# Performance work log

Measured on AMD Instinct MI355X. Metric: run time of the kernel, lower is better.

Reference implementation:

```python
import jax, jax.numpy as jnp
import numpy as np

B, M, IN, HID, A = 4096, 64, 3, 128, 64
D = 50.0                       # waveguide_bound
H_CONST = 5.0
PMAX = 10.0 ** (30 / 10 - 3)   # = 1.0 (30 dBm in Watts)
C_LIGHT = 3.0e8
FC = 6.0e9
DELTA_MIN = (C_LIGHT / FC) / 2.0  # 0.025
ALPHA = 0.2                    # LeakyReLU slope


def setup_inputs() -> dict:
    key = jax.random.key(0)
    ks = jax.random.split(key, 9)
    s = lambda k, sh: (jax.random.normal(k, sh, jnp.float32) * 0.1)
    return {
        "users": jax.random.normal(ks[0], (B, M, IN), jnp.float32),
        "W1": s(ks[1], (IN, HID)),    # GAT layer 1 projection (applied as h @ W)
        "a1": s(ks[2], (2 * HID,)),   # GAT layer 1 attention vector
        "W2": s(ks[3], (HID, HID)),   # GAT layer 2 projection
        "a2": s(ks[4], (2 * HID,)),
        "mw1": s(ks[5], (HID, 32)),   # MLP Linear(hidden, 32)
        "mb1": jnp.zeros((32,), jnp.float32),
        "mw2": s(ks[6], (32, 2 * A)), # MLP Linear(32, 2*num_antennas)
        "mb2": jnp.zeros((2 * A,), jnp.float32),
    }


def gat_layer(h, W, a):
    # Wh: [B, M, d]
    Wh = h @ W
    d = W.shape[1]
    # e[b,i,j] = leakyrelu( cat(Wh_i, Wh_j) . a ) = leakyrelu( Wh_i.a[:d] + Wh_j.a[d:] )
    si = Wh @ a[:d]          # [B, M]
    sj = Wh @ a[d:]          # [B, M]
    e = jax.nn.leaky_relu(si[:, :, None] + sj[:, None, :], ALPHA)  # [B, M, M]
    attn = jax.nn.softmax(e, axis=-1)  # softmax over neighbors j (dropout p=0 -> identity)
    h_prime = jnp.einsum('bij,bjd->bid', attn, Wh)
    return jax.nn.elu(h_prime)


def reference(users, W1, a1, W2, a2, mw1, mb1, mw2, mb2):
    h = gat_layer(users, W1, a1)
    h = gat_layer(h, W2, a2)
    pooled = jnp.max(h, axis=1)                      # [B, hidden]
    readout = jax.nn.relu(pooled @ mw1 + mb1) @ mw2 + mb2  # [B, 2A]
    raw_delta, raw_power = readout[:, :A], readout[:, A:]
    eps = 1e-6
    raw_delta = jax.nn.relu(raw_delta) + eps
    raw_power = jax.nn.relu(raw_power) + eps
    Bmax = 2.0 * D - (A - 1) * DELTA_MIN
    delta = Bmax * raw_delta / (jnp.sum(raw_delta, axis=1, keepdims=True) + eps)
    power = PMAX * raw_power / (jnp.sum(raw_power, axis=1, keepdims=True) + eps)
    return power, delta
```

## Files before the change

### kernel.cpp

```cpp
#include <hip/hip_runtime.h>

#define NBATCH 4096
#define OUT2 (NBATCH * 64)

typedef _Float16 f16;
typedef __attribute__((ext_vector_type(8))) _Float16 f16x8;
typedef __attribute__((ext_vector_type(4))) _Float16 f16x4;
typedef __attribute__((ext_vector_type(4))) float f32x4;

__device__ __forceinline__ float lrelu(float x) { return fmaxf(x, 0.2f * x); }
__device__ __forceinline__ float elu1(float x)  { return x > 0.0f ? x : __expf(x) - 1.0f; }
__device__ __forceinline__ void lds_fence() {
    asm volatile("s_waitcnt lgkmcnt(0)" ::: "memory");
}

__global__ void prep(const float* __restrict__ W2, const float* __restrict__ W1,
                     const float* __restrict__ a1, const float* __restrict__ a2,
                     f16* __restrict__ w2b, float* __restrict__ w1a, f16* __restrict__ w2ab) {
    const int flat = blockIdx.x * 256 + threadIdx.x;
    const int slot = flat >> 3, j = flat & 7;
    const int F2T = slot >> 8, kf = (slot >> 6) & 3, ln = slot & 63;
    const int lq = ln >> 4, lr = ln & 15;
    w2b[flat] = (f16)W2[(kf * 32 + lq * 8 + j) * 128 + F2T * 16 + lr];
    if (flat < 2048) {
        const int ks = flat >> 9, ln2 = (flat >> 3) & 63, jj = flat & 7;
        const int k = ks * 32 + ((ln2 >> 4) & 3) * 8 + jj;
        const int n = ln2 & 15;
        float v = 0.f;
        if (n < 2) {
            const float* av = a2 + n * 128;
            for (int f2 = 0; f2 < 128; ++f2) v = fmaf(W2[k * 128 + f2], av[f2], v);
        }
        w2ab[flat] = (f16)v;
    }
    if (flat >= 16381) {
        const int c = flat - 16381;
        float si = 0.f, sj = 0.f;
        for (int f = 0; f < 128; ++f) {
            const float w = W1[c * 128 + f];
            si = fmaf(w, a1[f], si);
            sj = fmaf(w, a1[128 + f], sj);
        }
        w1a[c] = si; w1a[3 + c] = sj;
    }
}

__global__ __launch_bounds__(256, 2)
void gat_kernel(const float* __restrict__ users,
                const float* __restrict__ W1,
                const f16* __restrict__ w2b,
                const float* __restrict__ w1a,
                const f16* __restrict__ w2ab,
                const float* __restrict__ mw1,
                const float* __restrict__ mb1,
                const float* __restrict__ mw2,
                const float* __restrict__ mb2,
                float* __restrict__ out)
{
    const int wid  = threadIdx.x >> 6;
    const int b    = blockIdx.x * 4 + wid;
    const int lane = threadIdx.x & 63;
    const int lr   = lane & 15;
    const int lq   = lane >> 4;

    __shared__ __align__(16) char smem[4 * 9344];
    char*  sw    = smem + wid * 9344;
    f16*   sMain = (f16*)sw;
    float* sSi   = (float*)(sw + 8192);
    float* sSj   = (float*)(sw + 8448);
    float* sPool = (float*)(sw + 8704);
    float* sHid  = (float*)(sw + 9216);

    const float* u = users + b * 192;

    {
        const float x = u[lane * 3], y = u[lane * 3 + 1], z = u[lane * 3 + 2];
        sSi[lane] = fmaf(x, w1a[0], fmaf(y, w1a[1], z * w1a[2]));
        sSj[lane] = fmaf(x, w1a[3], fmaf(y, w1a[4], z * w1a[5]));
    }
    lds_fence();

    f16x8 bfr[4];
    {
        float sjv[16];
        *(float4*)&sjv[0]  = *(const float4*)&sSj[lq * 8];
        *(float4*)&sjv[4]  = *(const float4*)&sSj[lq * 8 + 4];
        *(float4*)&sjv[8]  = *(const float4*)&sSj[32 + lq * 8];
        *(float4*)&sjv[12] = *(const float4*)&sSj[32 + lq * 8 + 4];
        f16x8 ap[4][2];
        #pragma unroll
        for (int mt = 0; mt < 4; ++mt) {
            const float si = sSi[mt * 16 + lr];
            float pv[16];
            float lsum = 0.f;
            #pragma unroll
            for (int jj = 0; jj < 8; ++jj) {
                const float t0 = si + sjv[jj];
                const float t1 = si + sjv[8 + jj];
                const float p0 = __expf(lrelu(t0));
                const float p1 = __expf(lrelu(t1));
                pv[jj] = p0; pv[8 + jj] = p1;
                lsum += p0 + p1;
            }
            lsum += __shfl_xor(lsum, 16, 64);
            lsum += __shfl_xor(lsum, 32, 64);
            const float inv = 1.0f / lsum;
            #pragma unroll
            for (int jj = 0; jj < 8; ++jj) {
                ap[mt][0][jj] = (f16)(pv[jj] * inv);
                ap[mt][1][jj] = (f16)(pv[8 + jj] * inv);
            }
        }
        f16x8 af2[2];
        #pragma unroll
        for (int ks = 0; ks < 2; ++ks) {
            #pragma unroll
            for (int jj = 0; jj < 8; ++jj) {
                const int node = ks * 32 + lq * 8 + jj;
                af2[ks][jj] = (lr < 3) ? (f16)u[node * 3 + lr] : (f16)0.f;
            }
        }
        #pragma unroll
        for (int nt = 0; nt < 4; ++nt) {
            f32x4 d1 = (f32x4){0.f, 0.f, 0.f, 0.f};
            d1 = __builtin_amdgcn_mfma_f32_16x16x32_f16(af2[0], ap[nt][0], d1, 0, 0, 0);
            d1 = __builtin_amdgcn_mfma_f32_16x16x32_f16(af2[1], ap[nt][1], d1, 0, 0, 0);
            const float c0 = __shfl(d1[0], lr, 64);
            const float c1 = __shfl(d1[1], lr, 64);
            const float c2 = __shfl(d1[2], lr, 64);
            #pragma unroll
            for (int jj = 0; jj < 8; ++jj) bfr[nt][jj] = (f16)0.f;
            if (lq == 0) {
                bfr[nt][0] = (f16)c0; bfr[nt][1] = (f16)c1; bfr[nt][2] = (f16)c2;
            }
        }
    }

    f16x8 hf[4][4];
    #pragma unroll
    for (int h = 0; h < 2; ++h) {
        #pragma unroll
        for (int ftl = 0; ftl < 4; ++ftl) {
            f16x8 af3;
            #pragma unroll
            for (int jj = 0; jj < 8; ++jj) af3[jj] = (f16)0.f;
            if (lq == 0) {
                #pragma unroll
                for (int jj = 0; jj < 3; ++jj)
                    af3[jj] = (f16)W1[jj * 128 + (h * 4 + ftl) * 16 + lr];
            }
            #pragma unroll
            for (int nt = 0; nt < 4; ++nt) {
                f32x4 acc = (f32x4){0.f, 0.f, 0.f, 0.f};
                acc = __builtin_amdgcn_mfma_f32_16x16x32_f16(af3, bfr[nt], acc, 0, 0, 0);
                f16x4 hv;
                #pragma unroll
                for (int r = 0; r < 4; ++r) hv[r] = (f16)elu1(acc[r]);
                const int n = nt * 16 + lr;
                const int gg = 2 * ftl + (lq >> 1);
                *(f16x4*)&sMain[n * 64 + ((gg ^ (n & 7)) << 3) + ((lq & 1) * 4)] = hv;
            }
        }
        lds_fence();
        #pragma unroll
        for (int nt = 0; nt < 4; ++nt) {
            const int n = nt * 16 + lr;
            #pragma unroll
            for (int ksl = 0; ksl < 2; ++ksl)
                hf[nt][h * 2 + ksl] =
                    *(const f16x8*)&sMain[n * 64 + (((ksl * 4 + lq) ^ (n & 7)) << 3)];
        }
        lds_fence();
    }

    {
        f32x4 sacc[4];
        #pragma unroll
        for (int mt = 0; mt < 4; ++mt) sacc[mt] = (f32x4){0.f, 0.f, 0.f, 0.f};
        #pragma unroll
        for (int ks = 0; ks < 4; ++ks) {
            f16x8 bsw = *(const f16x8*)(w2ab + (ks * 64 + lane) * 8);
            #pragma unroll
            for (int mt = 0; mt < 4; ++mt)
                sacc[mt] = __builtin_amdgcn_mfma_f32_16x16x32_f16(hf[mt][ks], bsw, sacc[mt], 0, 0, 0);
        }
        if (lr < 2) {
            float* dst = (lr == 0) ? sSi : sSj;
            #pragma unroll
            for (int mt = 0; mt < 4; ++mt)
                #pragma unroll
                for (int r = 0; r < 4; ++r)
                    dst[mt * 16 + lq * 4 + r] = sacc[mt][r];
        }
    }
    lds_fence();

    f16x8 bp[4][2];
    {
        float sjv[16];
        *(float4*)&sjv[0]  = *(const float4*)&sSj[lq * 8];
        *(float4*)&sjv[4]  = *(const float4*)&sSj[lq * 8 + 4];
        *(float4*)&sjv[8]  = *(const float4*)&sSj[32 + lq * 8];
        *(float4*)&sjv[12] = *(const float4*)&sSj[32 + lq * 8 + 4];
        #pragma unroll
        for (int mt = 0; mt < 4; ++mt) {
            const float si = sSi[mt * 16 + lr];
            float pv[16];
            float lsum = 0.f;
            #pragma unroll
            for (int jj = 0; jj < 8; ++jj) {
                const float t0 = si + sjv[jj];
                const float t1 = si + sjv[8 + jj];
                const float p0 = __expf(lrelu(t0));
                const float p1 = __expf(lrelu(t1));
                pv[jj] = p0; pv[8 + jj] = p1;
                lsum += p0 + p1;
            }
            lsum += __shfl_xor(lsum, 16, 64);
            lsum += __shfl_xor(lsum, 32, 64);
            const float inv = 1.0f / lsum;
            #pragma unroll
            for (int jj = 0; jj < 8; ++jj) {
                bp[mt][0][jj] = (f16)(pv[jj] * inv);
                bp[mt][1][jj] = (f16)(pv[8 + jj] * inv);
            }
        }
    }

    int fst[4];
    #pragma unroll
    for (int nt = 0; nt < 4; ++nt) {
        const int gg = nt * 2 + (lq >> 1);
        fst[nt] = lr * 64 + ((gg ^ (lr & 7)) << 3) + ((lq & 1) * 4);
    }
    const int er0 = lr * 64 + ((lq ^ (lr & 7)) << 3);
    const int er1 = lr * 64 + (((4 + lq) ^ (lr & 7)) << 3);

    {
        f16x8 bw2[4];
        #pragma unroll
        for (int kf = 0; kf < 4; ++kf)
            bw2[kf] = *(const f16x8*)(w2b + ((0 * 4 + kf) * 64 + lane) * 8);
        #pragma unroll
        for (int nt = 0; nt < 4; ++nt) {
            f32x4 acc = (f32x4){0.f, 0.f, 0.f, 0.f};
            #pragma unroll
            for (int kf = 0; kf < 4; ++kf)
                acc = __builtin_amdgcn_mfma_f32_16x16x32_f16(hf[nt][kf], bw2[kf], acc, 0, 0, 0);
            f16x4 hv;
            #pragma unroll
            for (int r = 0; r < 4; ++r) hv[r] = (f16)acc[r];
            *(f16x4*)&sMain[fst[nt]] = hv;
        }
    }
    lds_fence();

    #pragma unroll 1
    for (int ft = 0; ft < 8; ++ft) {
        f16* rb = sMain + ((ft & 1) << 10);
        if (ft < 7) {
            f16* wb = sMain + (((ft + 1) & 1) << 10);
            f16x8 bw2[4];
            #pragma unroll
            for (int kf = 0; kf < 4; ++kf)
                bw2[kf] = *(const f16x8*)(w2b + (((ft + 1) * 4 + kf) * 64 + lane) * 8);
            #pragma unroll
            for (int nt = 0; nt < 4; ++nt) {
                f32x4 acc = (f32x4){0.f, 0.f, 0.f, 0.f};
                #pragma unroll
                for (int kf = 0; kf < 4; ++kf)
                    acc = __builtin_amdgcn_mfma_f32_16x16x32_f16(hf[nt][kf], bw2[kf], acc, 0, 0, 0);
                f16x4 hv;
                #pragma unroll
                for (int r = 0; r < 4; ++r) hv[r] = (f16)acc[r];
                *(f16x4*)&wb[fst[nt]] = hv;
            }
        }

        f16x8 bh0 = *(const f16x8*)&rb[er0];
        f16x8 bh1 = *(const f16x8*)&rb[er1];
        float mx = -1e30f;
        #pragma unroll
        for (int mt = 0; mt < 4; ++mt) {
            f32x4 acc = (f32x4){0.f, 0.f, 0.f, 0.f};
            acc = __builtin_amdgcn_mfma_f32_16x16x32_f16(bp[mt][0], bh0, acc, 0, 0, 0);
            acc = __builtin_amdgcn_mfma_f32_16x16x32_f16(bp[mt][1], bh1, acc, 0, 0, 0);
            mx = fmaxf(mx, fmaxf(fmaxf(acc[0], acc[1]), fmaxf(acc[2], acc[3])));
        }
        mx = fmaxf(mx, __shfl_xor(mx, 16, 64));
        mx = fmaxf(mx, __shfl_xor(mx, 32, 64));
        if (lane < 16) sPool[ft * 16 + lane] = elu1(mx);
        lds_fence();
    }

    {
        const int o = lane & 31, hh = lane >> 5;
        float s0 = 0.f;
        #pragma unroll 8
        for (int kk = 0; kk < 64; ++kk) {
            const int c = hh * 64 + kk;
            s0 = fmaf(sPool[c], mw1[c * 32 + o], s0);
        }
        s0 += __shfl_xor(s0, 32, 64);
        if (lane < 32) sHid[lane] = fmaxf(s0 + mb1[o], 0.0f);
    }
    lds_fence();
    {
        float sA = mb2[lane], sB = mb2[64 + lane];
        #pragma unroll 8
        for (int q = 0; q < 32; ++q) {
            const float wA = mw2[q * 128 + lane];
            const float wB = mw2[q * 128 + 64 + lane];
            const float h0 = sHid[q];
            sA = fmaf(h0, wA, sA);  sB = fmaf(h0, wB, sB);
        }
        float rA = fmaxf(sA, 0.0f) + 1e-6f, rB = fmaxf(sB, 0.0f) + 1e-6f;
        float uA = rA, uB = rB;
        #pragma unroll
        for (int m = 1; m < 64; m <<= 1) {
            uA += __shfl_xor(uA, m, 64);  uB += __shfl_xor(uB, m, 64);
        }
        out[b * 64 + lane]        = rB / (uB + 1e-6f);
        out[OUT2 + b * 64 + lane] = 98.425f * rA / (uA + 1e-6f);
    }
}

extern "C" void kernel_launch(void* const* d_in, const int* in_sizes, int n_in,
                              void* d_out, int out_size, void* d_ws, size_t ws_size,
                              hipStream_t stream) {
    const float* users = (const float*)d_in[0];
    const float* W1    = (const float*)d_in[1];
    const float* a1    = (const float*)d_in[2];
    const float* W2    = (const float*)d_in[3];
    const float* a2    = (const float*)d_in[4];
    const float* mw1   = (const float*)d_in[5];
    const float* mb1   = (const float*)d_in[6];
    const float* mw2   = (const float*)d_in[7];
    const float* mb2   = (const float*)d_in[8];
    float* out = (float*)d_out;

    f16*   w2b  = (f16*)d_ws;
    float* w1a  = (float*)((char*)d_ws + 32768);
    f16*   w2ab = (f16*)((char*)d_ws + 32800);

    prep<<<64, 256, 0, stream>>>(W2, W1, a1, a2, w2b, w1a, w2ab);
    gat_kernel<<<NBATCH / 4, 256, 0, stream>>>(users, W1, w2b, w1a, w2ab,
                                               mw1, mb1, mw2, mb2, out);
}
```

Before: 114.7 us.

## Replace LDS transpose staging with register shuffles between MFMA stages

```diff
diff --git a/kernel.cpp b/kernel.cpp
--- a/kernel.cpp
+++ b/kernel.cpp
@@ -5,13 +5,35 @@
 
 typedef _Float16 f16;
 typedef __attribute__((ext_vector_type(8))) _Float16 f16x8;
-typedef __attribute__((ext_vector_type(4))) _Float16 f16x4;
 typedef __attribute__((ext_vector_type(4))) float f32x4;
 
 __device__ __forceinline__ float lrelu(float x) { return fmaxf(x, 0.2f * x); }
 __device__ __forceinline__ float elu1(float x)  { return x > 0.0f ? x : __expf(x) - 1.0f; }
 __device__ __forceinline__ void lds_fence() {
     asm volatile("s_waitcnt lgkmcnt(0)" ::: "memory");
+}
+__device__ __forceinline__ unsigned pk2(float a, float b) {
+    union { f16 h[2]; unsigned u; } t;
+    t.h[0] = (f16)a; t.h[1] = (f16)b;
+    return t.u;
+}
+__device__ __forceinline__ f16x8 xpose(unsigned p0l, unsigned p0h,
+                                       unsigned p1l, unsigned p1h,
+                                       int s0, int s1, bool hiSel) {
+    const unsigned a0l = (unsigned)__shfl((int)p0l, s0, 64);
+    const unsigned a0h = (unsigned)__shfl((int)p0h, s0, 64);
+    const unsigned b0l = (unsigned)__shfl((int)p0l, s1, 64);
+    const unsigned b0h = (unsigned)__shfl((int)p0h, s1, 64);
+    const unsigned a1l = (unsigned)__shfl((int)p1l, s0, 64);
+    const unsigned a1h = (unsigned)__shfl((int)p1h, s0, 64);
+    const unsigned b1l = (unsigned)__shfl((int)p1l, s1, 64);
+    const unsigned b1h = (unsigned)__shfl((int)p1h, s1, 64);
+    union { unsigned u[4]; f16x8 v; } o;
+    o.u[0] = hiSel ? a1l : a0l;
+    o.u[1] = hiSel ? a1h : a0h;
+    o.u[2] = hiSel ? b1l : b0l;
+    o.u[3] = hiSel ? b1h : b0h;
+    return o.v;
 }
 
 __global__ void prep(const float* __restrict__ W2, const float* __restrict__ W1,
@@ -62,14 +84,16 @@
     const int lane = threadIdx.x & 63;
     const int lr   = lane & 15;
     const int lq   = lane >> 4;
-
-    __shared__ __align__(16) char smem[4 * 9344];
-    char*  sw    = smem + wid * 9344;
-    f16*   sMain = (f16*)sw;
-    float* sSi   = (float*)(sw + 8192);
-    float* sSj   = (float*)(sw + 8448);
-    float* sPool = (float*)(sw + 8704);
-    float* sHid  = (float*)(sw + 9216);
+    const int s0   = (lane & 15) | ((lane & 16) << 1);
+    const int s1   = s0 + 16;
+    const bool hiSel = (lane & 32) != 0;
+
+    __shared__ __align__(16) char smem[4 * 1280];
+    char*  sw    = smem + wid * 1280;
+    float* sSi   = (float*)(sw);
+    float* sSj   = (float*)(sw + 256);
+    float* sPool = (float*)(sw + 512);
+    float* sHid  = (float*)(sw + 1024);
 
     const float* u = users + b * 192;
 
@@ -95,10 +119,8 @@
             float lsum = 0.f;
             #pragma unroll
             for (int jj = 0; jj < 8; ++jj) {
-                const float t0 = si + sjv[jj];
-                const float t1 = si + sjv[8 + jj];
-                const float p0 = __expf(lrelu(t0));
-                const float p1 = __expf(lrelu(t1));
+                const float p0 = __expf(lrelu(si + sjv[jj]));
+                const float p1 = __expf(lrelu(si + sjv[8 + jj]));
                 pv[jj] = p0; pv[8 + jj] = p1;
                 lsum += p0 + p1;
             }
@@ -140,37 +162,34 @@
     #pragma unroll
     for (int h = 0; h < 2; ++h) {
         #pragma unroll
-        for (int ftl = 0; ftl < 4; ++ftl) {
-            f16x8 af3;
-            #pragma unroll
-            for (int jj = 0; jj < 8; ++jj) af3[jj] = (f16)0.f;
-            if (lq == 0) {
+        for (int ksl = 0; ksl < 2; ++ksl) {
+            f32x4 acc[4][2];
+            #pragma unroll
+            for (int tp = 0; tp < 2; ++tp) {
+                const int ftl = 2 * ksl + tp;
+                f16x8 af3;
                 #pragma unroll
-                for (int jj = 0; jj < 3; ++jj)
-                    af3[jj] = (f16)W1[jj * 128 + (h * 4 + ftl) * 16 + lr];
+                for (int jj = 0; jj < 8; ++jj) af3[jj] = (f16)0.f;
+                if (lq == 0) {
+                    #pragma unroll
+                    for (int jj = 0; jj < 3; ++jj)
+                        af3[jj] = (f16)W1[jj * 128 + (h * 4 + ftl) * 16 + lr];
+                }
+                #pragma unroll
+                for (int nt = 0; nt < 4; ++nt) {
+                    acc[nt][tp] = (f32x4){0.f, 0.f, 0.f, 0.f};
+                    acc[nt][tp] = __builtin_amdgcn_mfma_f32_16x16x32_f16(af3, bfr[nt], acc[nt][tp], 0, 0, 0);
+                }
             }
             #pragma unroll
             for (int nt = 0; nt < 4; ++nt) {
-                f32x4 acc = (f32x4){0.f, 0.f, 0.f, 0.f};
-                acc = __builtin_amdgcn_mfma_f32_16x16x32_f16(af3, bfr[nt], acc, 0, 0, 0);
-                f16x4 hv;
-                #pragma unroll
-                for (int r = 0; r < 4; ++r) hv[r] = (f16)elu1(acc[r]);
-                const int n = nt * 16 + lr;
-                const int gg = 2 * ftl + (lq >> 1);
-                *(f16x4*)&sMain[n * 64 + ((gg ^ (n & 7)) << 3) + ((lq & 1) * 4)] = hv;
-            }
-        }
-        lds_fence();
-        #pragma unroll
-        for (int nt = 0; nt < 4; ++nt) {
-            const int n = nt * 16 + lr;
-            #pragma unroll
-            for (int ksl = 0; ksl < 2; ++ksl)
-                hf[nt][h * 2 + ksl] =
-                    *(const f16x8*)&sMain[n * 64 + (((ksl * 4 + lq) ^ (n & 7)) << 3)];
-        }
-        lds_fence();
+                const unsigned p0l = pk2(elu1(acc[nt][0][0]), elu1(acc[nt][0][1]));
+                const unsigned p0h = pk2(elu1(acc[nt][0][2]), elu1(acc[nt][0][3]));
+                const unsigned p1l = pk2(elu1(acc[nt][1][0]), elu1(acc[nt][1][1]));
+                const unsigned p1h = pk2(elu1(acc[nt][1][2]), elu1(acc[nt][1][3]));
+                hf[nt][h * 2 + ksl] = xpose(p0l, p0h, p1l, p1h, s0, s1, hiSel);
+            }
+        }
     }
 
     {
@@ -184,6 +203,7 @@
             for (int mt = 0; mt < 4; ++mt)
                 sacc[mt] = __builtin_amdgcn_mfma_f32_16x16x32_f16(hf[mt][ks], bsw, sacc[mt], 0, 0, 0);
         }
+        lds_fence();
         if (lr < 2) {
             float* dst = (lr == 0) ? sSi : sSj;
             #pragma unroll
@@ -209,10 +229,8 @@
             float lsum = 0.f;
             #pragma unroll
             for (int jj = 0; jj < 8; ++jj) {
-                const float t0 = si + sjv[jj];
-                const float t1 = si + sjv[8 + jj];
-                const float p0 = __expf(lrelu(t0));
-                const float p1 = __expf(lrelu(t1));
+                const float p0 = __expf(lrelu(si + sjv[jj]));
+                const float p1 = __expf(lrelu(si + sjv[8 + jj]));
                 pv[jj] = p0; pv[8 + jj] = p1;
                 lsum += p0 + p1;
             }
@@ -227,58 +245,25 @@
         }
     }
 
-    int fst[4];
-    #pragma unroll
-    for (int nt = 0; nt < 4; ++nt) {
-        const int gg = nt * 2 + (lq >> 1);
-        fst[nt] = lr * 64 + ((gg ^ (lr & 7)) << 3) + ((lq & 1) * 4);
-    }
-    const int er0 = lr * 64 + ((lq ^ (lr & 7)) << 3);
-    const int er1 = lr * 64 + (((4 + lq) ^ (lr & 7)) << 3);
-
-    {
+    #pragma unroll 1
+    for (int ft = 0; ft < 8; ++ft) {
         f16x8 bw2[4];
         #pragma unroll
         for (int kf = 0; kf < 4; ++kf)
-            bw2[kf] = *(const f16x8*)(w2b + ((0 * 4 + kf) * 64 + lane) * 8);
+            bw2[kf] = *(const f16x8*)(w2b + ((ft * 4 + kf) * 64 + lane) * 8);
+        unsigned pkq[4][2];
         #pragma unroll
         for (int nt = 0; nt < 4; ++nt) {
             f32x4 acc = (f32x4){0.f, 0.f, 0.f, 0.f};
             #pragma unroll
             for (int kf = 0; kf < 4; ++kf)
                 acc = __builtin_amdgcn_mfma_f32_16x16x32_f16(hf[nt][kf], bw2[kf], acc, 0, 0, 0);
-            f16x4 hv;
-            #pragma unroll
-            for (int r = 0; r < 4; ++r) hv[r] = (f16)acc[r];
-            *(f16x4*)&sMain[fst[nt]] = hv;
-        }
-    }
-    lds_fence();
-
-    #pragma unroll 1
-    for (int ft = 0; ft < 8; ++ft) {
-        f16* rb = sMain + ((ft & 1) << 10);
-        if (ft < 7) {
-            f16* wb = sMain + (((ft + 1) & 1) << 10);
-            f16x8 bw2[4];
-            #pragma unroll
-            for (int kf = 0; kf < 4; ++kf)
-                bw2[kf] = *(const f16x8*)(w2b + (((ft + 1) * 4 + kf) * 64 + lane) * 8);
-            #pragma unroll
-            for (int nt = 0; nt < 4; ++nt) {
-                f32x4 acc = (f32x4){0.f, 0.f, 0.f, 0.f};
-                #pragma unroll
-                for (int kf = 0; kf < 4; ++kf)
-                    acc = __builtin_amdgcn_mfma_f32_16x16x32_f16(hf[nt][kf], bw2[kf], acc, 0, 0, 0);
-                f16x4 hv;
-                #pragma unroll
-                for (int r = 0; r < 4; ++r) hv[r] = (f16)acc[r];
-                *(f16x4*)&wb[fst[nt]] = hv;
-            }
-        }
-
-        f16x8 bh0 = *(const f16x8*)&rb[er0];
-        f16x8 bh1 = *(const f16x8*)&rb[er1];
+            pkq[nt][0] = pk2(acc[0], acc[1]);
+            pkq[nt][1] = pk2(acc[2], acc[3]);
+        }
+        const f16x8 bh0 = xpose(pkq[0][0], pkq[0][1], pkq[1][0], pkq[1][1], s0, s1, hiSel);
+        const f16x8 bh1 = xpose(pkq[2][0], pkq[2][1], pkq[3][0], pkq[3][1], s0, s1, hiSel);
+
         float mx = -1e30f;
         #pragma unroll
         for (int mt = 0; mt < 4; ++mt) {
@@ -290,19 +275,19 @@
         mx = fmaxf(mx, __shfl_xor(mx, 16, 64));
         mx = fmaxf(mx, __shfl_xor(mx, 32, 64));
         if (lane < 16) sPool[ft * 16 + lane] = elu1(mx);
-        lds_fence();
-    }
+    }
+    lds_fence();
 
     {
         const int o = lane & 31, hh = lane >> 5;
-        float s0 = 0.f;
+        float s0r = 0.f;
         #pragma unroll 8
         for (int kk = 0; kk < 64; ++kk) {
             const int c = hh * 64 + kk;
-            s0 = fmaf(sPool[c], mw1[c * 32 + o], s0);
-        }
-        s0 += __shfl_xor(s0, 32, 64);
-        if (lane < 32) sHid[lane] = fmaxf(s0 + mb1[o], 0.0f);
+            s0r = fmaf(sPool[c], mw1[c * 32 + o], s0r);
+        }
+        s0r += __shfl_xor(s0r, 32, 64);
+        if (lane < 32) sHid[lane] = fmaxf(s0r + mb1[o], 0.0f);
     }
     lds_fence();
     {
```

After: 114.4 us. Within noise of the previous version (-0.2%).
